# Optimization experiments

Measured on AMD Instinct MI355X. Metric: run time of the kernel, lower is better.

The kernel has to match this reference:

```python
import jax, jax.numpy as jnp
import numpy as np

D_MODEL = 1024
H = 16
DK = 64
DV = 64
EPS = 1e-5


def setup_inputs() -> dict:
    key = jax.random.key(0)
    ks = jax.random.split(key, 12)
    B, NQ, NK = 4, 2048, 2048
    std = 0.001  # init.normal_(weight, std=0.001), biases zero
    return {
        "queries": jax.random.normal(ks[0], (B, NQ, D_MODEL), jnp.float32),
        "keys": jax.random.normal(ks[1], (B, NK, D_MODEL), jnp.float32),
        "values": jax.random.normal(ks[2], (B, NK, D_MODEL), jnp.float32),
        "attention_mask": jnp.ones((B, NK), jnp.int32),  # 1 = keep
        "Wq": jax.random.normal(ks[3], (D_MODEL, H * DK), jnp.float32) * std,
        "bq": jnp.zeros((H * DK,), jnp.float32),
        "Wk": jax.random.normal(ks[4], (D_MODEL, H * DK), jnp.float32) * std,
        "bk": jnp.zeros((H * DK,), jnp.float32),
        "Wv": jax.random.normal(ks[5], (D_MODEL, H * DV), jnp.float32) * std,
        "bv": jnp.zeros((H * DV,), jnp.float32),
        "Wo": jax.random.normal(ks[6], (H * DV, D_MODEL), jnp.float32) * std,
        "bo": jnp.zeros((D_MODEL,), jnp.float32),
        "gamma": jnp.ones((D_MODEL,), jnp.float32),
        "beta": jnp.zeros((D_MODEL,), jnp.float32),
    }


def reference(queries, keys, values, attention_mask, Wq, bq, Wk, bk, Wv, bv, Wo, bo, gamma, beta):
    b, nq, _ = queries.shape
    nk = keys.shape[1]
    q = (queries @ Wq + bq).reshape(b, nq, H, DK)   # (b, nq, h, dk)
    k = (keys @ Wk + bk).reshape(b, nk, H, DK)      # (b, nk, h, dk)
    v = (values @ Wv + bv).reshape(b, nk, H, DV)    # (b, nk, h, dv)
    scale = 1.0 / np.sqrt(DK).astype(np.float32)
    att = jnp.einsum('bqhd,bkhd->bhqk', q, k) * scale  # (b, h, nq, nk)
    mask = attention_mask[:, None, None, :].astype(bool)
    att = jnp.where(mask, att, -jnp.inf)
    att = jax.nn.softmax(att, axis=-1)
    # dropout is identity at inference
    out = jnp.einsum('bhqk,bkhd->bqhd', att, v).reshape(b, nq, H * DV)
    out = out @ Wo + bo
    x = out + queries  # residual
    mean = jnp.mean(x, axis=-1, keepdims=True)
    var = jnp.mean(jnp.square(x - mean), axis=-1, keepdims=True)
    return gamma * (x - mean) * jax.lax.rsqrt(var + EPS) + beta
```

## Files before the change

kernel.cpp:

```cpp
#include <hip/hip_runtime.h>

typedef __bf16 bf16x8 __attribute__((ext_vector_type(8)));
typedef __bf16 bf16x4 __attribute__((ext_vector_type(4)));
typedef float f32x4 __attribute__((ext_vector_type(4)));
typedef unsigned short u16;

#if __has_builtin(__builtin_amdgcn_exp2f)
#define EXP2(x) __builtin_amdgcn_exp2f(x)
#else
#define EXP2(x) exp2f(x)
#endif

__device__ __forceinline__ float bf2f(u16 u){
    union { unsigned int i; float f; } x; x.i = ((unsigned int)u) << 16; return x.f;
}
__device__ __forceinline__ u16 bfbits(float f){
    __bf16 h = (__bf16)f;
    union { __bf16 b; u16 u; } x; x.b = h; return x.u;
}
__device__ __forceinline__ int4 cvt8(const float4 a, const float4 b){
    union { __bf16 h[8]; int4 v; } u;
    u.h[0] = (__bf16)a.x; u.h[1] = (__bf16)a.y; u.h[2] = (__bf16)a.z; u.h[3] = (__bf16)a.w;
    u.h[4] = (__bf16)b.x; u.h[5] = (__bf16)b.y; u.h[6] = (__bf16)b.z; u.h[7] = (__bf16)b.w;
    return u.v;
}
__device__ __forceinline__ void gload_lds16(const void* g, void* l){
    __builtin_amdgcn_global_load_lds(
        (const __attribute__((address_space(1))) unsigned int*)g,
        (__attribute__((address_space(3))) unsigned int*)l, 16, 0, 0);
}

__global__ __launch_bounds__(256) void transpose4(
    const float* __restrict__ w0, const float* __restrict__ w1,
    const float* __restrict__ w2, const float* __restrict__ w3,
    u16* __restrict__ out)
{
    __shared__ float tile[32][33];
    int mat = blockIdx.z;
    const float* in = (mat == 0) ? w0 : (mat == 1) ? w1 : (mat == 2) ? w2 : w3;
    u16* o = out + (size_t)mat * 1048576;
    int bx = blockIdx.x * 32, by = blockIdx.y * 32;
    int tx = threadIdx.x & 31, ty = threadIdx.x >> 5;
    #pragma unroll
    for (int i = 0; i < 32; i += 8)
        tile[ty + i][tx] = in[(size_t)(by + ty + i) * 1024 + bx + tx];
    __syncthreads();
    #pragma unroll
    for (int i = 0; i < 32; i += 8)
        o[(size_t)(bx + ty + i) * 1024 + by + tx] = bfbits(tile[tx][ty + i]);
}

__global__ __launch_bounds__(256) void gemm_qkv(
    const float* __restrict__ Aq, const float* __restrict__ Ak,
    const float* __restrict__ Avv, const u16* __restrict__ Wt3,
    const float* __restrict__ bq, const float* __restrict__ bk,
    const float* __restrict__ bv,
    u16* __restrict__ Qp, u16* __restrict__ Kp, u16* __restrict__ Vtd,
    float qscale)
{
    constexpr int K = 1024;
    __shared__ alignas(16) u16 smem[16384];
    char* const AB = (char*)smem;
    auto Abase = [&](int buf){ return AB + buf * 8192; };
    auto Bbase = [&](int buf){ return AB + 16384 + buf * 8192; };

    const int tid = threadIdx.x;
    const int lane = tid & 63, wid = tid >> 6;
    const int wm = wid >> 1, wn = wid & 1;

    const int wg = blockIdx.x;
    const int seg = wg >> 9;
    const int w = wg & 511;
    const int xcd = w & 7, rest = w >> 3;
    const int ntile = rest & 7, mhi = rest >> 3;
    const int m0 = (mhi * 8 + xcd) * 128;
    const int n0 = ntile * 128;

    const float* A = (seg == 0) ? Aq : (seg == 1) ? Ak : Avv;
    const u16* Bt = Wt3 + (size_t)seg * 1048576;
    const float* bias = (seg == 0) ? bq : (seg == 1) ? bk : bv;
    const float scale = (seg == 0) ? qscale : 1.0f;
    u16* Cv = (seg == 0) ? Qp : (seg == 1) ? Kp : Vtd;
    const bool vmode = (seg == 2);

    const int r0 = tid >> 2;
    const int kc = (tid & 3) * 8;
    const int kcB = (tid & 3) * 16;
    const int fr = lane & 15;
    const int fkB = (lane >> 4) * 16;

    const float* Af0 = A + (size_t)(m0 + r0) * K + kc;
    const float* Af1 = Af0 + (size_t)64 * K;

    const int srow = lane >> 2;
    auto stageB = [&](int buf, int tcol) {
        #pragma unroll
        for (int i = 0; i < 2; i++) {
            int rt = wid * 32 + i * 16;
            int r = rt + srow;
            gload_lds16(Bt + (size_t)(n0 + r) * K + tcol + ((lane & 3) ^ (r & 3)) * 8,
                        Bbase(buf) + rt * 64);
        }
    };
    const int aswz = ((r0 & 3) << 4);

    stageB(0, 0);
    {
        int4 w0v = cvt8(((const float4*)Af0)[0], ((const float4*)Af0)[1]);
        int4 w1v = cvt8(((const float4*)Af1)[0], ((const float4*)Af1)[1]);
        *(int4*)(Abase(0) + r0 * 64 + (kcB ^ aswz)) = w0v;
        *(int4*)(Abase(0) + (r0 + 64) * 64 + (kcB ^ aswz)) = w1v;
    }
    __syncthreads();

    f32x4 acc[4][4] = {};
    constexpr int NT = K / 32;
    for (int t = 0; t < NT; ++t) {
        const int cur = t & 1, nxt = cur ^ 1;
        float4 a00, a01, a10, a11;
        if (t + 1 < NT) {
            stageB(nxt, (t + 1) * 32);
            a00 = ((const float4*)(Af0 + (t + 1) * 32))[0];
            a01 = ((const float4*)(Af0 + (t + 1) * 32))[1];
            a10 = ((const float4*)(Af1 + (t + 1) * 32))[0];
            a11 = ((const float4*)(Af1 + (t + 1) * 32))[1];
        }
        bf16x8 af[4], bfr[4];
        #pragma unroll
        for (int i = 0; i < 4; i++) {
            int ra = wm * 64 + i * 16 + fr;
            int rb = wn * 64 + i * 16 + fr;
            af[i]  = *(const bf16x8*)(Abase(cur) + ra * 64 + (fkB ^ ((ra & 3) << 4)));
            bfr[i] = *(const bf16x8*)(Bbase(cur) + rb * 64 + (fkB ^ ((rb & 3) << 4)));
        }
        #pragma unroll
        for (int mi = 0; mi < 4; mi++)
            #pragma unroll
            for (int ni = 0; ni < 4; ni++)
                acc[mi][ni] = __builtin_amdgcn_mfma_f32_16x16x32_bf16(
                    af[mi], bfr[ni], acc[mi][ni], 0, 0, 0);
        if (t + 1 < NT) {
            *(int4*)(Abase(nxt) + r0 * 64 + (kcB ^ aswz)) = cvt8(a00, a01);
            *(int4*)(Abase(nxt) + (r0 + 64) * 64 + (kcB ^ aswz)) = cvt8(a10, a11);
        }
        __syncthreads();
    }

    char* const CtB = AB;
    #pragma unroll
    for (int ni = 0; ni < 4; ni++) {
        int nn = wn * 64 + ni * 16 + fr;
        float bcol = bias[n0 + nn];
        #pragma unroll
        for (int mi = 0; mi < 4; mi++) {
            #pragma unroll
            for (int r = 0; r < 4; r++) {
                int mm = wm * 64 + mi * 16 + (lane >> 4) * 4 + r;
                float val = (acc[mi][ni][r] + bcol) * scale;
                int row  = vmode ? nn : mm;
                int colb = (vmode ? mm : nn) * 2;
                *(u16*)(CtB + row * 256 +
                        ((colb & 15) | ((((colb >> 4)) ^ (row & 7)) << 4))) = bfbits(val);
            }
        }
    }
    __syncthreads();
    #pragma unroll
    for (int p = 0; p < 8; p++) {
        int idx = p * 256 + tid;
        int row = idx >> 4, ck = idx & 15;
        int4 val = *(const int4*)(CtB + row * 256 + ((ck ^ (row & 7)) << 4));
        if (vmode) {
            int n = n0 + row, m = m0 + ck * 8;
            int h = n >> 6, d = n & 63, bb = m >> 11, q = m & 2047;
            *(int4*)&Cv[(size_t)(bb * 16 + h) * 131072 + (size_t)d * 2048 + q] = val;
        } else {
            int m = m0 + row, n = n0 + ck * 8;
            int h = n >> 6, d = n & 63, bb = m >> 11, q = m & 2047;
            *(int4*)&Cv[(size_t)(bb * 16 + h) * 131072 + (size_t)q * 64 + d] = val;
        }
    }
}

__global__ __launch_bounds__(256) void gemm_o(
    const u16* __restrict__ Ah, const u16* __restrict__ Bt,
    const float* __restrict__ bias, const float* __restrict__ resid,
    u16* __restrict__ Cv)
{
    constexpr int K = 1024;
    __shared__ alignas(16) u16 smem[16384];
    char* const AB = (char*)smem;
    auto Abase = [&](int buf){ return AB + buf * 8192; };
    auto Bbase = [&](int buf){ return AB + 16384 + buf * 8192; };

    const int tid = threadIdx.x;
    const int lane = tid & 63, wid = tid >> 6;
    const int wm = wid >> 1, wn = wid & 1;

    const int wg = blockIdx.x;
    const int xcd = wg & 7, rest = wg >> 3;
    const int ntile = rest & 7, mhi = rest >> 3;
    const int m0 = (mhi * 8 + xcd) * 128;
    const int n0 = ntile * 128;

    const int fr = lane & 15;
    const int fkB = (lane >> 4) * 16;

    const int srow = lane >> 2;
    auto stageB = [&](int buf, int tcol) {
        #pragma unroll
        for (int i = 0; i < 2; i++) {
            int rt = wid * 32 + i * 16;
            int r = rt + srow;
            gload_lds16(Bt + (size_t)(n0 + r) * K + tcol + ((lane & 3) ^ (r & 3)) * 8,
                        Bbase(buf) + rt * 64);
        }
    };
    auto stageA = [&](int buf, int tcol) {
        #pragma unroll
        for (int i = 0; i < 2; i++) {
            int rt = wid * 32 + i * 16;
            int r = rt + srow;
            gload_lds16(Ah + (size_t)(m0 + r) * K + tcol + ((lane & 3) ^ (r & 3)) * 8,
                        Abase(buf) + rt * 64);
        }
    };

    stageB(0, 0);
    stageA(0, 0);
    __syncthreads();

    f32x4 acc[4][4] = {};
    constexpr int NT = K / 32;
    for (int t = 0; t < NT; ++t) {
        const int cur = t & 1, nxt = cur ^ 1;
        if (t + 1 < NT) {
            stageB(nxt, (t + 1) * 32);
            stageA(nxt, (t + 1) * 32);
        }
        bf16x8 af[4], bfr[4];
        #pragma unroll
        for (int i = 0; i < 4; i++) {
            int ra = wm * 64 + i * 16 + fr;
            int rb = wn * 64 + i * 16 + fr;
            af[i]  = *(const bf16x8*)(Abase(cur) + ra * 64 + (fkB ^ ((ra & 3) << 4)));
            bfr[i] = *(const bf16x8*)(Bbase(cur) + rb * 64 + (fkB ^ ((rb & 3) << 4)));
        }
        #pragma unroll
        for (int mi = 0; mi < 4; mi++)
            #pragma unroll
            for (int ni = 0; ni < 4; ni++)
                acc[mi][ni] = __builtin_amdgcn_mfma_f32_16x16x32_bf16(
                    af[mi], bfr[ni], acc[mi][ni], 0, 0, 0);
        __syncthreads();
    }

    char* const CtB = AB;
    #pragma unroll
    for (int ni = 0; ni < 4; ni++) {
        int nn = wn * 64 + ni * 16 + fr;
        float bcol = bias[n0 + nn];
        #pragma unroll
        for (int mi = 0; mi < 4; mi++) {
            #pragma unroll
            for (int r = 0; r < 4; r++) {
                int mm = wm * 64 + mi * 16 + (lane >> 4) * 4 + r;
                float val = acc[mi][ni][r] + bcol + resid[(size_t)(m0 + mm) * 1024 + n0 + nn];
                int colb = nn * 2;
                *(u16*)(CtB + mm * 256 +
                        ((colb & 15) | ((((colb >> 4)) ^ (mm & 7)) << 4))) = bfbits(val);
            }
        }
    }
    __syncthreads();
    #pragma unroll
    for (int p = 0; p < 8; p++) {
        int idx = p * 256 + tid;
        int row = idx >> 4, ck = idx & 15;
        int4 val = *(const int4*)(CtB + row * 256 + ((ck ^ (row & 7)) << 4));
        *(int4*)&Cv[(size_t)(m0 + row) * 1024 + n0 + ck * 8] = val;
    }
}

__global__ __launch_bounds__(256, 4) void attn_k(
    const u16* __restrict__ Qp, const u16* __restrict__ Kp,
    const u16* __restrict__ Vt, const int* __restrict__ mask,
    u16* __restrict__ O)
{
    __shared__ alignas(16) u16 Ks[2][64][64];
    __shared__ alignas(16) u16 Vs[2][64][64];
    __shared__ alignas(16) u16 Pl[4][16][64];

    const int wg = blockIdx.x;
    const int xc = wg & 7;
    const int rm = wg >> 3;
    const int qx = rm & 15;
    const int bh = (rm >> 4) * 8 + xc;
    const int b = bh >> 4, h = bh & 15;
    const int q0 = qx * 128;
    const int tid = threadIdx.x, wid = tid >> 6, lane = tid & 63;
    const int ql = lane & 15, g = lane >> 4;
    const int qw = q0 + wid * 32;

    const u16* Qbh = Qp + (size_t)bh * 131072;
    const u16* Kbh = Kp + (size_t)bh * 131072;
    const u16* Vbh = Vt + (size_t)bh * 131072;
    const int* mrow = mask + b * 2048;

    char* KsB0 = (char*)Ks;
    char* VsB0 = (char*)Vs;
    char* PlB = (char*)Pl + wid * 2048;

    bf16x8 qf[2][2];
    #pragma unroll
    for (int fi = 0; fi < 2; fi++)
        #pragma unroll
        for (int ks = 0; ks < 2; ks++)
            qf[fi][ks] = *(const bf16x8*)&Qbh[(size_t)(qw + fi * 16 + ql) * 64 + ks * 32 + g * 8];

    f32x4 oacc[2][4] = {};
    float lrow[2] = {0.f, 0.f};
    const f32x4 kZero = {0.f, 0.f, 0.f, 0.f};

    int pwoff[4], proff[2];
    #pragma unroll
    for (int kb = 0; kb < 4; kb++)
        pwoff[kb] = ql * 128 + ((kb * 32 + g * 8) ^ ((ql & 7) << 4));
    #pragma unroll
    for (int ks = 0; ks < 2; ks++)
        proff[ks] = ql * 128 + ((ks * 64 + g * 16) ^ ((ql & 7) << 4));

    const int lrow8 = lane >> 3;
    const int coff  = ((lane & 7) ^ lrow8) << 4;
    const int rb    = wid * 16;

    auto stage = [&](int buf, int tt) {
        const size_t kv0 = (size_t)tt * 64;
        #pragma unroll
        for (int i = 0; i < 2; i++) {
            const int rt = rb + i * 8;
            gload_lds16((const char*)Kbh + (kv0 + rt + lrow8) * 128 + coff,
                        KsB0 + buf * 8192 + rt * 128);
            gload_lds16((const char*)Vbh + (size_t)(rt + lrow8) * 4096 + kv0 * 2 + coff,
                        VsB0 + buf * 8192 + rt * 128);
        }
    };

    stage(0, 0);
    int mcur = mrow[lane];
    __syncthreads();

    for (int t = 0; t < 32; ++t) {
        const int cur = t & 1, nxt = cur ^ 1;
        char* KsB = KsB0 + cur * 8192;
        char* VsB = VsB0 + cur * 8192;
        int mnxt = 1;
        if (t < 31) {
            stage(nxt, t + 1);
            mnxt = mrow[(t + 1) * 64 + lane];
        }
        const bool anym = (__ballot(mcur == 0) != 0ull);

        bf16x8 pf[2][2];
        #pragma unroll
        for (int fi = 0; fi < 2; fi++) {
            float ts = 0.f;
            __builtin_amdgcn_s_setprio(1);
            #pragma unroll
            for (int kb = 0; kb < 4; kb++) {
                const int row = kb * 16 + ql;
                const int swz = (row & 7) << 4;
                bf16x8 kf0 = *(const bf16x8*)(KsB + row * 128 + ((g * 16) ^ swz));
                bf16x8 kf1 = *(const bf16x8*)(KsB + row * 128 + ((64 + g * 16) ^ swz));
                f32x4 a = __builtin_amdgcn_mfma_f32_16x16x32_bf16(kf0, qf[fi][0], kZero, 0, 0, 0);
                a = __builtin_amdgcn_mfma_f32_16x16x32_bf16(kf1, qf[fi][1], a, 0, 0, 0);
                if (anym) {
                    int4 mi = *(const int4*)&mrow[t * 64 + kb * 16 + g * 4];
                    a[0] += mi.x ? 0.f : -1e30f;
                    a[1] += mi.y ? 0.f : -1e30f;
                    a[2] += mi.z ? 0.f : -1e30f;
                    a[3] += mi.w ? 0.f : -1e30f;
                }
                float p0 = EXP2(a[0]);
                float p1 = EXP2(a[1]);
                float p2 = EXP2(a[2]);
                float p3 = EXP2(a[3]);
                ts += (p0 + p1) + (p2 + p3);
                bf16x4 pb;
                pb[0] = (__bf16)p0; pb[1] = (__bf16)p1;
                pb[2] = (__bf16)p2; pb[3] = (__bf16)p3;
                *(bf16x4*)(PlB + pwoff[kb]) = pb;
            }
            __builtin_amdgcn_s_setprio(0);
            lrow[fi] += ts;
            pf[fi][0] = *(const bf16x8*)(PlB + proff[0]);
            pf[fi][1] = *(const bf16x8*)(PlB + proff[1]);
        }

        __builtin_amdgcn_s_setprio(1);
        #pragma unroll
        for (int dt = 0; dt < 4; dt++) {
            int row = dt * 16 + ql;
            int swz = (row & 7) << 4;
            bf16x8 vf0 = *(const bf16x8*)(VsB + row * 128 + ((g * 16) ^ swz));
            bf16x8 vf1 = *(const bf16x8*)(VsB + row * 128 + ((64 + g * 16) ^ swz));
            #pragma unroll
            for (int fi = 0; fi < 2; fi++) {
                oacc[fi][dt] = __builtin_amdgcn_mfma_f32_16x16x32_bf16(vf0, pf[fi][0], oacc[fi][dt], 0, 0, 0);
                oacc[fi][dt] = __builtin_amdgcn_mfma_f32_16x16x32_bf16(vf1, pf[fi][1], oacc[fi][dt], 0, 0, 0);
            }
        }
        __builtin_amdgcn_s_setprio(0);

        mcur = mnxt;
        __syncthreads();
    }

    #pragma unroll
    for (int fi = 0; fi < 2; fi++) {
        lrow[fi] += __shfl_xor(lrow[fi], 16, 64);
        lrow[fi] += __shfl_xor(lrow[fi], 32, 64);
        float inv = 1.f / lrow[fi];
        #pragma unroll
        for (int dt = 0; dt < 4; dt++) {
            bf16x4 ob;
            ob[0] = (__bf16)(oacc[fi][dt][0] * inv);
            ob[1] = (__bf16)(oacc[fi][dt][1] * inv);
            ob[2] = (__bf16)(oacc[fi][dt][2] * inv);
            ob[3] = (__bf16)(oacc[fi][dt][3] * inv);
            *(bf16x4*)(PlB + ql * 128 + ((dt * 32 + g * 8) ^ ((ql & 7) << 4))) = ob;
        }
        int rr = lane >> 2;
        int q = qw + fi * 16 + rr;
        #pragma unroll
        for (int pass = 0; pass < 2; pass++) {
            int cc = (lane & 3) + pass * 4;
            int4 val = *(const int4*)(PlB + rr * 128 + ((cc * 16) ^ ((rr & 7) << 4)));
            *(int4*)&O[((size_t)(b * 2048 + q)) * 1024 + h * 64 + cc * 8] = val;
        }
    }
}

__global__ __launch_bounds__(256) void ln_k(
    const u16* __restrict__ X, const float* __restrict__ gamma,
    const float* __restrict__ beta, float* __restrict__ out)
{
    const int row = blockIdx.x, tid = threadIdx.x;
    ushort4 u = ((const ushort4*)(X + (size_t)row * 1024))[tid];
    float v0 = bf2f(u.x), v1 = bf2f(u.y), v2 = bf2f(u.z), v3 = bf2f(u.w);
    float s = (v0 + v1) + (v2 + v3);
    float s2 = (v0 * v0 + v1 * v1) + (v2 * v2 + v3 * v3);
    #pragma unroll
    for (int off = 1; off < 64; off <<= 1) {
        s  += __shfl_xor(s, off, 64);
        s2 += __shfl_xor(s2, off, 64);
    }
    __shared__ float ss[4], ss2[4];
    int wid = tid >> 6;
    if ((tid & 63) == 0) { ss[wid] = s; ss2[wid] = s2; }
    __syncthreads();
    s = ss[0] + ss[1] + ss[2] + ss[3];
    s2 = ss2[0] + ss2[1] + ss2[2] + ss2[3];
    float mean = s * (1.f / 1024.f);
    float var = s2 * (1.f / 1024.f) - mean * mean;
    float rstd = rsqrtf(var + 1e-5f);
    float4 gm = ((const float4*)gamma)[tid];
    float4 be = ((const float4*)beta)[tid];
    float4 o;
    o.x = (v0 - mean) * rstd * gm.x + be.x;
    o.y = (v1 - mean) * rstd * gm.y + be.y;
    o.z = (v2 - mean) * rstd * gm.z + be.z;
    o.w = (v3 - mean) * rstd * gm.w + be.w;
    ((float4*)(out + (size_t)row * 1024))[tid] = o;
}

extern "C" void kernel_launch(void* const* d_in, const int* in_sizes, int n_in,
                              void* d_out, int out_size, void* d_ws, size_t ws_size,
                              hipStream_t stream)
{
    const float* queries = (const float*)d_in[0];
    const float* keys    = (const float*)d_in[1];
    const float* values  = (const float*)d_in[2];
    const int*   mask    = (const int*)d_in[3];
    const float* Wq = (const float*)d_in[4];
    const float* bq = (const float*)d_in[5];
    const float* Wk = (const float*)d_in[6];
    const float* bk = (const float*)d_in[7];
    const float* Wv = (const float*)d_in[8];
    const float* bv = (const float*)d_in[9];
    const float* Wo = (const float*)d_in[10];
    const float* bo = (const float*)d_in[11];
    const float* gamma = (const float*)d_in[12];
    const float* beta  = (const float*)d_in[13];

    u16* ws = (u16*)d_ws;
    u16* Wt = ws;
    u16* Qp = ws + 4 * 1048576;
    u16* Kp = Qp + 8388608;
    u16* Vt = Kp + 8388608;
    u16* O  = Vt + 8388608;
    u16* X  = Qp;

    const float qscale = 0.125f * 1.44269504088896f;

    transpose4<<<dim3(32, 32, 4), 256, 0, stream>>>(Wq, Wk, Wv, Wo, Wt);
    gemm_qkv<<<dim3(1536), 256, 0, stream>>>(queries, keys, values, Wt,
                                             bq, bk, bv, Qp, Kp, Vt, qscale);
    attn_k<<<dim3(1024), 256, 0, stream>>>(Qp, Kp, Vt, mask, O);
    gemm_o<<<dim3(512), 256, 0, stream>>>(O, Wt + 3145728, bo, queries, X);
    ln_k<<<8192, 256, 0, stream>>>(X, gamma, beta, (float*)d_out);
}
```

Measured before the change: 218.5 us.

## Pre-convert QKV activations to bf16 and use async LDS-loading bf16 GEMM

Adds a separate kernel that converts the fp32 queries, keys and values to bf16 in workspace. A new QKV GEMM then streams bf16 A tiles straight into LDS with direct global-to-LDS loads instead of converting fp32 inside the GEMM, and sets a launch-bounds occupancy hint. This is meant to remove the in-loop fp32 load and convert cost and halve the A-tile bytes the GEMM reads. In exchange it adds an extra pass that reads and writes the whole activation tensors. The path is used only when the workspace is large enough, otherwise the old fp32 path runs.

```diff
diff --git a/kernel.cpp b/kernel.cpp
--- a/kernel.cpp
+++ b/kernel.cpp
@@ -50,7 +50,141 @@
         o[(size_t)(bx + ty + i) * 1024 + by + tx] = bfbits(tile[tx][ty + i]);
 }
 
-__global__ __launch_bounds__(256) void gemm_qkv(
+__global__ __launch_bounds__(256) void cvt_a(
+    const float* __restrict__ q, const float* __restrict__ k,
+    const float* __restrict__ v, u16* __restrict__ out)
+{
+    const int bid = blockIdx.x;
+    const int seg = bid >> 12;
+    const float* src = (seg == 0) ? q : (seg == 1) ? k : v;
+    u16* dst = out + (size_t)seg * 8388608;
+    const size_t off = (size_t)(bid & 4095) * 2048 + threadIdx.x * 8;
+    float4 a = *(const float4*)(src + off);
+    float4 b = *(const float4*)(src + off + 4);
+    *(int4*)(dst + off) = cvt8(a, b);
+}
+
+__global__ __launch_bounds__(256, 4) void gemm_qkv_bf16(
+    const u16* __restrict__ Ah3, const u16* __restrict__ Wt3,
+    const float* __restrict__ bq, const float* __restrict__ bk,
+    const float* __restrict__ bv,
+    u16* __restrict__ Qp, u16* __restrict__ Kp, u16* __restrict__ Vtd,
+    float qscale)
+{
+    constexpr int K = 1024;
+    __shared__ alignas(16) u16 smem[16384];
+    char* const AB = (char*)smem;
+    auto Abase = [&](int buf){ return AB + buf * 8192; };
+    auto Bbase = [&](int buf){ return AB + 16384 + buf * 8192; };
+
+    const int tid = threadIdx.x;
+    const int lane = tid & 63, wid = tid >> 6;
+    const int wm = wid >> 1, wn = wid & 1;
+
+    const int wg = blockIdx.x;
+    const int seg = wg >> 9;
+    const int w = wg & 511;
+    const int xcd = w & 7, rest = w >> 3;
+    const int ntile = rest & 7, mhi = rest >> 3;
+    const int m0 = (mhi * 8 + xcd) * 128;
+    const int n0 = ntile * 128;
+
+    const u16* A  = Ah3 + (size_t)seg * 8388608;
+    const u16* Bt = Wt3 + (size_t)seg * 1048576;
+    const float* bias = (seg == 0) ? bq : (seg == 1) ? bk : bv;
+    const float scale = (seg == 0) ? qscale : 1.0f;
+    u16* Cv = (seg == 0) ? Qp : (seg == 1) ? Kp : Vtd;
+    const bool vmode = (seg == 2);
+
+    const int fr = lane & 15;
+    const int fkB = (lane >> 4) * 16;
+
+    const int srow = lane >> 2;
+    auto stageB = [&](int buf, int tcol) {
+        #pragma unroll
+        for (int i = 0; i < 2; i++) {
+            int rt = wid * 32 + i * 16;
+            int r = rt + srow;
+            gload_lds16(Bt + (size_t)(n0 + r) * K + tcol + ((lane & 3) ^ (r & 3)) * 8,
+                        Bbase(buf) + rt * 64);
+        }
+    };
+    auto stageA = [&](int buf, int tcol) {
+        #pragma unroll
+        for (int i = 0; i < 2; i++) {
+            int rt = wid * 32 + i * 16;
+            int r = rt + srow;
+            gload_lds16(A + (size_t)(m0 + r) * K + tcol + ((lane & 3) ^ (r & 3)) * 8,
+                        Abase(buf) + rt * 64);
+        }
+    };
+
+    stageB(0, 0);
+    stageA(0, 0);
+    __syncthreads();
+
+    f32x4 acc[4][4] = {};
+    constexpr int NT = K / 32;
+    for (int t = 0; t < NT; ++t) {
+        const int cur = t & 1, nxt = cur ^ 1;
+        if (t + 1 < NT) {
+            stageB(nxt, (t + 1) * 32);
+            stageA(nxt, (t + 1) * 32);
+        }
+        bf16x8 af[4], bfr[4];
+        #pragma unroll
+        for (int i = 0; i < 4; i++) {
+            int ra = wm * 64 + i * 16 + fr;
+            int rb = wn * 64 + i * 16 + fr;
+            af[i]  = *(const bf16x8*)(Abase(cur) + ra * 64 + (fkB ^ ((ra & 3) << 4)));
+            bfr[i] = *(const bf16x8*)(Bbase(cur) + rb * 64 + (fkB ^ ((rb & 3) << 4)));
+        }
+        #pragma unroll
+        for (int mi = 0; mi < 4; mi++)
+            #pragma unroll
+            for (int ni = 0; ni < 4; ni++)
+                acc[mi][ni] = __builtin_amdgcn_mfma_f32_16x16x32_bf16(
+                    af[mi], bfr[ni], acc[mi][ni], 0, 0, 0);
+        __syncthreads();
+    }
+
+    char* const CtB = AB;
+    #pragma unroll
+    for (int ni = 0; ni < 4; ni++) {
+        int nn = wn * 64 + ni * 16 + fr;
+        float bcol = bias[n0 + nn];
+        #pragma unroll
+        for (int mi = 0; mi < 4; mi++) {
+            #pragma unroll
+            for (int r = 0; r < 4; r++) {
+                int mm = wm * 64 + mi * 16 + (lane >> 4) * 4 + r;
+                float val = (acc[mi][ni][r] + bcol) * scale;
+                int row  = vmode ? nn : mm;
+                int colb = (vmode ? mm : nn) * 2;
+                *(u16*)(CtB + row * 256 +
+                        ((colb & 15) | ((((colb >> 4)) ^ (row & 7)) << 4))) = bfbits(val);
+            }
+        }
+    }
+    __syncthreads();
+    #pragma unroll
+    for (int p = 0; p < 8; p++) {
+        int idx = p * 256 + tid;
+        int row = idx >> 4, ck = idx & 15;
+        int4 val = *(const int4*)(CtB + row * 256 + ((ck ^ (row & 7)) << 4));
+        if (vmode) {
+            int n = n0 + row, m = m0 + ck * 8;
+            int h = n >> 6, d = n & 63, bb = m >> 11, q = m & 2047;
+            *(int4*)&Cv[(size_t)(bb * 16 + h) * 131072 + (size_t)d * 2048 + q] = val;
+        } else {
+            int m = m0 + row, n = n0 + ck * 8;
+            int h = n >> 6, d = n & 63, bb = m >> 11, q = m & 2047;
+            *(int4*)&Cv[(size_t)(bb * 16 + h) * 131072 + (size_t)q * 64 + d] = val;
+        }
+    }
+}
+
+__global__ __launch_bounds__(256) void gemm_qkv_f32(
     const float* __restrict__ Aq, const float* __restrict__ Ak,
     const float* __restrict__ Avv, const u16* __restrict__ Wt3,
     const float* __restrict__ bq, const float* __restrict__ bk,
@@ -494,19 +628,37 @@
     const float* beta  = (const float*)d_in[13];
 
     u16* ws = (u16*)d_ws;
-    u16* Wt = ws;
-    u16* Qp = ws + 4 * 1048576;
-    u16* Kp = Qp + 8388608;
-    u16* Vt = Kp + 8388608;
-    u16* O  = Vt + 8388608;
-    u16* X  = Qp;
-
     const float qscale = 0.125f * 1.44269504088896f;
 
-    transpose4<<<dim3(32, 32, 4), 256, 0, stream>>>(Wq, Wk, Wv, Wo, Wt);
-    gemm_qkv<<<dim3(1536), 256, 0, stream>>>(queries, keys, values, Wt,
-                                             bq, bk, bv, Qp, Kp, Vt, qscale);
-    attn_k<<<dim3(1024), 256, 0, stream>>>(Qp, Kp, Vt, mask, O);
-    gemm_o<<<dim3(512), 256, 0, stream>>>(O, Wt + 3145728, bo, queries, X);
-    ln_k<<<8192, 256, 0, stream>>>(X, gamma, beta, (float*)d_out);
-}
+    if (ws_size >= 109051904ull) {
+        u16* Wt  = ws;
+        u16* Ah3 = ws + 4194304;
+        u16* Qp  = ws + 29360128;
+        u16* Kp  = Qp + 8388608;
+        u16* Vt  = Kp + 8388608;
+        u16* O   = Ah3;
+        u16* X   = Qp;
+
+        transpose4<<<dim3(32, 32, 4), 256, 0, stream>>>(Wq, Wk, Wv, Wo, Wt);
+        cvt_a<<<dim3(12288), 256, 0, stream>>>(queries, keys, values, Ah3);
+        gemm_qkv_bf16<<<dim3(1536), 256, 0, stream>>>(Ah3, Wt, bq, bk, bv,
+                                                      Qp, Kp, Vt, qscale);
+        attn_k<<<dim3(1024), 256, 0, stream>>>(Qp, Kp, Vt, mask, O);
+        gemm_o<<<dim3(512), 256, 0, stream>>>(O, Wt + 3145728, bo, queries, X);
+        ln_k<<<8192, 256, 0, stream>>>(X, gamma, beta, (float*)d_out);
+    } else {
+        u16* Wt = ws;
+        u16* Qp = ws + 4 * 1048576;
+        u16* Kp = Qp + 8388608;
+        u16* Vt = Kp + 8388608;
+        u16* O  = Vt + 8388608;
+        u16* X  = Qp;
+
+        transpose4<<<dim3(32, 32, 4), 256, 0, stream>>>(Wq, Wk, Wv, Wo, Wt);
+        gemm_qkv_f32<<<dim3(1536), 256, 0, stream>>>(queries, keys, values, Wt,
+                                                     bq, bk, bv, Qp, Kp, Vt, qscale);
+        attn_k<<<dim3(1024), 256, 0, stream>>>(Qp, Kp, Vt, mask, O);
+        gemm_o<<<dim3(512), 256, 0, stream>>>(O, Wt + 3145728, bo, queries, X);
+        ln_k<<<8192, 256, 0, stream>>>(X, gamma, beta, (float*)d_out);
+    }
+}
```

New measurement: 222.7 us. About the same (+1.9%).
